# Performance work log

Measured on AMD Instinct MI355X. Metric: run time of the kernel, lower is better.

Reference implementation:

```python
import jax, jax.numpy as jnp
import numpy as np

N = 8_000_000   # hits
P = 100_000     # particle ids (0 = noise)


def setup_inputs() -> dict:
    key = jax.random.key(0)
    k1, k2, k3, k4, k5 = jax.random.split(key, 5)
    return {
        "w": jax.random.uniform(k1, (N,), dtype=jnp.float32),
        "beta": jax.random.uniform(k2, (N,), dtype=jnp.float32),
        "x": jax.random.normal(k3, (N, 3), dtype=jnp.float32),
        "y": jax.random.normal(k4, (N,), dtype=jnp.float32),
        "particle_id": jax.random.randint(k5, (N,), 0, P),
        "num_pids": P,
    }


def reference(w, beta, x, y, particle_id, num_pids):
    # BackgroundLoss.forward: only beta and particle_id matter; sb = 0.1.
    sb = jnp.asarray(0.1, beta.dtype)
    pid = particle_id

    # Per-particle max beta (segmented max replaces the per-pid argmax loop).
    counts = jax.ops.segment_sum(jnp.ones_like(beta), pid, num_segments=num_pids)
    max_beta = jax.ops.segment_max(beta, pid, num_segments=num_pids)

    # torch.unique(particle_id[particle_id > 0]) -> pids > 0 that actually occur.
    seg_ids = jnp.arange(num_pids)
    valid = (counts > 0) & (seg_ids > 0)
    n_valid = jnp.maximum(jnp.sum(valid), 1)
    attractive = jnp.sum(jnp.where(valid, 1.0 - max_beta, 0.0)) / n_valid.astype(beta.dtype)

    # Noise (pid == 0) term: sb * sum(n * beta) / nb.
    noise_mask = (pid == 0).astype(beta.dtype)
    nb = jnp.sum(noise_mask)
    noise = sb * jnp.sum(noise_mask * beta) / jnp.maximum(nb, 1.0)

    # If there are no noise hits the original returns 0.
    return jnp.where(nb == 0, jnp.asarray(0.0, beta.dtype), attractive + noise)
```

## Files before the change

### kernel.cpp

```cpp
#include <hip/hip_runtime.h>


#define ACC_NOISE  0
#define ACC_NB     1
#define ACC_ATTR   2
#define ACC_NVALID 3

#define RANGE_BITS_BIG 15
#define RANGE_BIG      (1 << RANGE_BITS_BIG)
#define NRANGE_BIG     4
#define TPB_BIG        1024

#define RANGE_BITS 14
#define RANGE      (1 << RANGE_BITS)
#define NRANGE     8
#define TPB        512

#define BPR        64

__global__ void bg_init_acc(float* __restrict__ acc) {
    if (threadIdx.x < 4) acc[threadIdx.x] = 0.0f;
}


__global__ __launch_bounds__(TPB_BIG) void bg_main_big(
        const float* __restrict__ beta, const int* __restrict__ pid,
        float* __restrict__ acc, unsigned int* __restrict__ slabs, int n) {
    extern __shared__ unsigned int tbl[];
    const int r = blockIdx.x / BPR;
    const int b = blockIdx.x % BPR;
    const int lo = r << RANGE_BITS_BIG;

    for (int i = threadIdx.x; i < RANGE_BIG; i += TPB_BIG) tbl[i] = 0u;
    __syncthreads();

    float noise_local = 0.0f;
    int nb_local = 0;

    const int n4 = n >> 2;
    const float4* __restrict__ b4 = (const float4*)beta;
    const int4* __restrict__ p4 = (const int4*)pid;
    const int gtid = b * TPB_BIG + (int)threadIdx.x;
    const int gstride = BPR * TPB_BIG;

    auto proc = [&](int p, float v) {
        int d = p - lo;
        if ((unsigned)d < (unsigned)RANGE_BIG) {
            if (p == 0) {
                noise_local += v;
                nb_local += 1;
            } else {
                unsigned int bits = __float_as_uint(v) + 1u;
                if (bits > tbl[d]) atomicMax(&tbl[d], bits);
            }
        }
    };

    int i = gtid;
    for (; i + gstride < n4; i += 2 * gstride) {
        float4 bb0 = b4[i];           int4 pp0 = p4[i];
        float4 bb1 = b4[i + gstride]; int4 pp1 = p4[i + gstride];
        proc(pp0.x, bb0.x); proc(pp0.y, bb0.y);
        proc(pp0.z, bb0.z); proc(pp0.w, bb0.w);
        proc(pp1.x, bb1.x); proc(pp1.y, bb1.y);
        proc(pp1.z, bb1.z); proc(pp1.w, bb1.w);
    }
    if (i < n4) {
        float4 bb = b4[i]; int4 pp = p4[i];
        proc(pp.x, bb.x); proc(pp.y, bb.y);
        proc(pp.z, bb.z); proc(pp.w, bb.w);
    }
    if (b == 0) {
        for (int t = (n4 << 2) + (int)threadIdx.x; t < n; t += TPB_BIG)
            proc(pid[t], beta[t]);
    }

    #pragma unroll
    for (int off = 32; off > 0; off >>= 1) {
        noise_local += __shfl_down(noise_local, off);
        nb_local    += __shfl_down(nb_local, off);
    }
    if ((threadIdx.x & 63) == 0 && nb_local != 0) {
        atomicAdd(&acc[ACC_NOISE], noise_local);
        atomicAdd(&acc[ACC_NB], (float)nb_local);
    }

    __syncthreads();
    uint4* __restrict__ o4 = (uint4*)(slabs + (size_t)blockIdx.x * RANGE_BIG);
    const uint4* __restrict__ t4 = (const uint4*)tbl;
    for (int k = threadIdx.x; k < RANGE_BIG / 4; k += TPB_BIG) o4[k] = t4[k];
}


__global__ __launch_bounds__(TPB) void bg_main_lds(
        const float* __restrict__ beta, const int* __restrict__ pid,
        float* __restrict__ acc, unsigned int* __restrict__ slabs, int n) {
    __shared__ unsigned int tbl[RANGE];
    const int r = blockIdx.x / BPR;
    const int b = blockIdx.x % BPR;
    const int lo = r << RANGE_BITS;

    for (int i = threadIdx.x; i < RANGE; i += TPB) tbl[i] = 0u;
    __syncthreads();

    float noise_local = 0.0f;
    int nb_local = 0;

    const int n4 = n >> 2;
    const float4* __restrict__ b4 = (const float4*)beta;
    const int4* __restrict__ p4 = (const int4*)pid;
    const int gtid = b * TPB + (int)threadIdx.x;
    const int gstride = BPR * TPB;

    auto proc = [&](int p, float v) {
        int d = p - lo;
        if ((unsigned)d < (unsigned)RANGE) {
            if (p == 0) {
                noise_local += v;
                nb_local += 1;
            } else {
                unsigned int bits = __float_as_uint(v) + 1u;
                if (bits > tbl[d]) atomicMax(&tbl[d], bits);
            }
        }
    };

    int i = gtid;
    for (; i + gstride < n4; i += 2 * gstride) {
        float4 bb0 = b4[i];           int4 pp0 = p4[i];
        float4 bb1 = b4[i + gstride]; int4 pp1 = p4[i + gstride];
        proc(pp0.x, bb0.x); proc(pp0.y, bb0.y);
        proc(pp0.z, bb0.z); proc(pp0.w, bb0.w);
        proc(pp1.x, bb1.x); proc(pp1.y, bb1.y);
        proc(pp1.z, bb1.z); proc(pp1.w, bb1.w);
    }
    if (i < n4) {
        float4 bb = b4[i]; int4 pp = p4[i];
        proc(pp.x, bb.x); proc(pp.y, bb.y);
        proc(pp.z, bb.z); proc(pp.w, bb.w);
    }
    if (b == 0) {
        for (int t = (n4 << 2) + (int)threadIdx.x; t < n; t += TPB)
            proc(pid[t], beta[t]);
    }

    #pragma unroll
    for (int off = 32; off > 0; off >>= 1) {
        noise_local += __shfl_down(noise_local, off);
        nb_local    += __shfl_down(nb_local, off);
    }
    if ((threadIdx.x & 63) == 0 && nb_local != 0) {
        atomicAdd(&acc[ACC_NOISE], noise_local);
        atomicAdd(&acc[ACC_NB], (float)nb_local);
    }

    __syncthreads();
    uint4* __restrict__ o4 = (uint4*)(slabs + (size_t)blockIdx.x * RANGE);
    const uint4* __restrict__ t4 = (const uint4*)tbl;
    for (int k = threadIdx.x; k < RANGE / 4; k += TPB) o4[k] = t4[k];
}


template <int RBITS>
__global__ __launch_bounds__(256) void bg_reduce_slab_t(
        const unsigned int* __restrict__ slabs, float* __restrict__ acc,
        const int* __restrict__ num_pids_p) {
    const int RSZ = 1 << RBITS;
    const int P = *num_pids_p;
    const int t = blockIdx.x * 256 + (int)threadIdx.x;
    const int e = t & (RSZ - 1);
    const int r = t >> RBITS;

    unsigned int v = 0u;
    const unsigned int* __restrict__ base =
        slabs + (size_t)(r * BPR) * RSZ + e;
    #pragma unroll 4
    for (int b = 0; b < BPR; ++b) {
        unsigned int u = base[(size_t)b * RSZ];
        v = (u > v) ? u : v;
    }

    const int p = (r << RBITS) | e;
    float s = 0.0f;
    int c = 0;
    if (p > 0 && p < P && v != 0u) {
        s = 1.0f - __uint_as_float(v - 1u);
        c = 1;
    }
    #pragma unroll
    for (int off = 32; off > 0; off >>= 1) {
        s += __shfl_down(s, off);
        c += __shfl_down(c, off);
    }
    if ((threadIdx.x & 63) == 0 && (c != 0 || s != 0.0f)) {
        atomicAdd(&acc[ACC_ATTR], s);
        atomicAdd(&acc[ACC_NVALID], (float)c);
    }
}


__global__ void bg_init(float* __restrict__ acc,
                        unsigned int* __restrict__ max_bits,
                        const int* __restrict__ num_pids_p) {
    const int P = *num_pids_p;
    const int gstride = gridDim.x * blockDim.x;
    const int tid = blockIdx.x * blockDim.x + threadIdx.x;
    if (tid < 4) acc[tid] = 0.0f;
    for (int i = tid; i < P; i += gstride) max_bits[i] = 0u;
}

__global__ void bg_main(const float* __restrict__ beta,
                        const int* __restrict__ pid,
                        float* __restrict__ acc,
                        unsigned int* __restrict__ max_bits, int n) {
    const int gstride = gridDim.x * blockDim.x;
    const int tid = blockIdx.x * blockDim.x + threadIdx.x;
    const int n4 = n >> 2;
    float noise_local = 0.0f;
    int nb_local = 0;
    auto proc = [&](int p, float b) {
        if (p == 0) { noise_local += b; nb_local += 1; }
        else {
            unsigned int bits = __float_as_uint(b) + 1u;
            if (bits > max_bits[p]) atomicMax(&max_bits[p], bits);
        }
    };
    const float4* __restrict__ b4 = (const float4*)beta;
    const int4* __restrict__ p4 = (const int4*)pid;
    for (int i = tid; i < n4; i += gstride) {
        float4 b = b4[i]; int4 p = p4[i];
        proc(p.x, b.x); proc(p.y, b.y); proc(p.z, b.z); proc(p.w, b.w);
    }
    for (int i = (n4 << 2) + tid; i < n; i += gstride)
        proc(pid[i], beta[i]);
    #pragma unroll
    for (int off = 32; off > 0; off >>= 1) {
        noise_local += __shfl_down(noise_local, off);
        nb_local    += __shfl_down(nb_local, off);
    }
    if ((threadIdx.x & 63) == 0 && nb_local != 0) {
        atomicAdd(&acc[ACC_NOISE], noise_local);
        atomicAdd(&acc[ACC_NB], (float)nb_local);
    }
}

__global__ void bg_reduce(const unsigned int* __restrict__ max_bits,
                          float* __restrict__ acc,
                          const int* __restrict__ num_pids_p) {
    const int P = *num_pids_p;
    const int gstride = gridDim.x * blockDim.x;
    float s = 0.0f;
    int c = 0;
    for (int i = blockIdx.x * blockDim.x + threadIdx.x; i < P; i += gstride) {
        if (i == 0) continue;
        unsigned int v = max_bits[i];
        if (v != 0u) { s += 1.0f - __uint_as_float(v - 1u); c += 1; }
    }
    #pragma unroll
    for (int off = 32; off > 0; off >>= 1) {
        s += __shfl_down(s, off);
        c += __shfl_down(c, off);
    }
    if ((threadIdx.x & 63) == 0 && (c != 0 || s != 0.0f)) {
        atomicAdd(&acc[ACC_ATTR], s);
        atomicAdd(&acc[ACC_NVALID], (float)c);
    }
}


__global__ void bg_finalize(const float* __restrict__ acc,
                            float* __restrict__ out) {
    float nb = acc[ACC_NB];
    float n_valid = fmaxf(acc[ACC_NVALID], 1.0f);
    float attractive = acc[ACC_ATTR] / n_valid;
    float noise = 0.1f * acc[ACC_NOISE] / fmaxf(nb, 1.0f);
    out[0] = (nb == 0.0f) ? 0.0f : (attractive + noise);
}

extern "C" void kernel_launch(void* const* d_in, const int* in_sizes, int n_in,
                              void* d_out, int out_size, void* d_ws, size_t ws_size,
                              hipStream_t stream) {
    const float* beta = (const float*)d_in[1];
    const int* pid = (const int*)d_in[4];
    const int* num_pids_p = (const int*)d_in[5];
    const int n = in_sizes[1];

    float* acc = (float*)d_ws;
    float* out = (float*)d_out;

    const size_t slab_bytes = (size_t)NRANGE * BPR * RANGE * sizeof(unsigned int);

    if (ws_size >= 16 + slab_bytes) {
        unsigned int* slabs = (unsigned int*)((char*)d_ws + 16);

        bool big = (hipFuncSetAttribute(
                        (const void*)bg_main_big,
                        hipFuncAttributeMaxDynamicSharedMemorySize,
                        RANGE_BIG * (int)sizeof(unsigned int)) == hipSuccess);

        bg_init_acc<<<1, 64, 0, stream>>>(acc);
        if (big) {
            bg_main_big<<<NRANGE_BIG * BPR, TPB_BIG,
                          RANGE_BIG * sizeof(unsigned int), stream>>>(
                beta, pid, acc, slabs, n);
            bg_reduce_slab_t<RANGE_BITS_BIG>
                <<<(NRANGE_BIG * RANGE_BIG) / 256, 256, 0, stream>>>(
                    slabs, acc, num_pids_p);
        } else {
            bg_main_lds<<<NRANGE * BPR, TPB, 0, stream>>>(beta, pid, acc, slabs, n);
            bg_reduce_slab_t<RANGE_BITS>
                <<<(NRANGE * RANGE) / 256, 256, 0, stream>>>(
                    slabs, acc, num_pids_p);
        }
        bg_finalize<<<1, 1, 0, stream>>>(acc, out);
    } else {
        unsigned int* max_bits = (unsigned int*)((char*)d_ws + 16);
        bg_init<<<512, 256, 0, stream>>>(acc, max_bits, num_pids_p);
        bg_main<<<2048, 256, 0, stream>>>(beta, pid, acc, max_bits, n);
        bg_reduce<<<512, 256, 0, stream>>>(max_bits, acc, num_pids_p);
        bg_finalize<<<1, 1, 0, stream>>>(acc, out);
    }
}
```

Measured before the change: 249.1 us.

## Cut pid ranges from four to three by folding tail range into range zero

Adds a new path that splits the pid space into three 32K ranges instead of four. The small tail above 3*32K (up to 4096 ids) is handled in an extra LDS table owned by the range-0 blocks. It raises blocks per range to 85 so all 255 blocks still cover the device. The goal is fewer full passes over the beta/pid arrays, since each range reads the whole input. In exchange range-0 blocks do more per-element work and LDS use grows, and the tail table silently assumes num_pids is at most 3*32768+4096.

```diff
diff --git a/kernel.cpp b/kernel.cpp
--- a/kernel.cpp
+++ b/kernel.cpp
@@ -6,20 +6,161 @@
 #define ACC_ATTR   2
 #define ACC_NVALID 3
 
-#define RANGE_BITS_BIG 15
-#define RANGE_BIG      (1 << RANGE_BITS_BIG)
-#define NRANGE_BIG     4
-#define TPB_BIG        1024
+#define RB          15
+#define RANGE_BIG   (1 << RB)
+#define NR_MAIN     3
+#define HI_BASE     (NR_MAIN << RB)
+#define HI_RANGE    4096
+#define BPR_BIG     85
+#define TPB_BIG     1024
+
+#define NRANGE_BIG  4
+#define BPR         64
 
 #define RANGE_BITS 14
 #define RANGE      (1 << RANGE_BITS)
 #define NRANGE     8
 #define TPB        512
 
-#define BPR        64
-
 __global__ void bg_init_acc(float* __restrict__ acc) {
     if (threadIdx.x < 4) acc[threadIdx.x] = 0.0f;
+}
+
+
+__global__ __launch_bounds__(TPB_BIG) void bg_main_r3(
+        const float* __restrict__ beta, const int* __restrict__ pid,
+        float* __restrict__ acc, unsigned int* __restrict__ slabs,
+        unsigned int* __restrict__ hi_slabs, int n) {
+    extern __shared__ unsigned int tbl[];
+    unsigned int* __restrict__ hi = tbl + RANGE_BIG;
+    const int r = blockIdx.x / BPR_BIG;
+    const int b = blockIdx.x % BPR_BIG;
+    const int lo = r << RB;
+
+    for (int i = threadIdx.x; i < RANGE_BIG + HI_RANGE; i += TPB_BIG) tbl[i] = 0u;
+    __syncthreads();
+
+    float noise_local = 0.0f;
+    int nb_local = 0;
+
+    const int n4 = n >> 2;
+    const float4* __restrict__ b4 = (const float4*)beta;
+    const int4* __restrict__ p4 = (const int4*)pid;
+    const int gtid = b * TPB_BIG + (int)threadIdx.x;
+    const int gstride = BPR_BIG * TPB_BIG;
+
+    auto stream = [&](auto&& proc) {
+        int i = gtid;
+        for (; i + gstride < n4; i += 2 * gstride) {
+            float4 bb0 = b4[i];           int4 pp0 = p4[i];
+            float4 bb1 = b4[i + gstride]; int4 pp1 = p4[i + gstride];
+            proc(pp0.x, bb0.x); proc(pp0.y, bb0.y);
+            proc(pp0.z, bb0.z); proc(pp0.w, bb0.w);
+            proc(pp1.x, bb1.x); proc(pp1.y, bb1.y);
+            proc(pp1.z, bb1.z); proc(pp1.w, bb1.w);
+        }
+        if (i < n4) {
+            float4 bb = b4[i]; int4 pp = p4[i];
+            proc(pp.x, bb.x); proc(pp.y, bb.y);
+            proc(pp.z, bb.z); proc(pp.w, bb.w);
+        }
+    };
+
+    if (r == 0) {
+        auto proc0 = [&](int p, float v) {
+            if (p == 0) { noise_local += v; nb_local += 1; return; }
+            unsigned int bits = __float_as_uint(v) + 1u;
+            if ((unsigned)p < (unsigned)RANGE_BIG) {
+                if (bits > tbl[p]) atomicMax(&tbl[p], bits);
+            } else {
+                int d = p - HI_BASE;
+                if ((unsigned)d < (unsigned)HI_RANGE)
+                    if (bits > hi[d]) atomicMax(&hi[d], bits);
+            }
+        };
+        stream(proc0);
+        if (b == 0) {
+            for (int t = (n4 << 2) + (int)threadIdx.x; t < n; t += TPB_BIG)
+                proc0(pid[t], beta[t]);
+        }
+    } else {
+        auto proc = [&](int p, float v) {
+            int d = p - lo;
+            if ((unsigned)d < (unsigned)RANGE_BIG) {
+                unsigned int bits = __float_as_uint(v) + 1u;
+                if (bits > tbl[d]) atomicMax(&tbl[d], bits);
+            }
+        };
+        stream(proc);
+    }
+
+    #pragma unroll
+    for (int off = 32; off > 0; off >>= 1) {
+        noise_local += __shfl_down(noise_local, off);
+        nb_local    += __shfl_down(nb_local, off);
+    }
+    if ((threadIdx.x & 63) == 0 && nb_local != 0) {
+        atomicAdd(&acc[ACC_NOISE], noise_local);
+        atomicAdd(&acc[ACC_NB], (float)nb_local);
+    }
+
+    __syncthreads();
+    uint4* __restrict__ o4 = (uint4*)(slabs + (size_t)blockIdx.x * RANGE_BIG);
+    const uint4* __restrict__ t4 = (const uint4*)tbl;
+    for (int k = threadIdx.x; k < RANGE_BIG / 4; k += TPB_BIG) o4[k] = t4[k];
+    if (r == 0) {
+        uint4* __restrict__ h4 = (uint4*)(hi_slabs + (size_t)b * HI_RANGE);
+        const uint4* __restrict__ hs4 = (const uint4*)hi;
+        for (int k = threadIdx.x; k < HI_RANGE / 4; k += TPB_BIG) h4[k] = hs4[k];
+    }
+}
+
+__global__ __launch_bounds__(256) void bg_reduce_r3(
+        const unsigned int* __restrict__ slabs,
+        const unsigned int* __restrict__ hi_slabs,
+        float* __restrict__ acc, const int* __restrict__ num_pids_p) {
+    const int P = *num_pids_p;
+    const int t = blockIdx.x * 256 + (int)threadIdx.x;
+
+    unsigned int v = 0u;
+    int p;
+    if (t < NR_MAIN * RANGE_BIG) {
+        const int e = t & (RANGE_BIG - 1);
+        const int r = t >> RB;
+        const unsigned int* __restrict__ base =
+            slabs + (size_t)(r * BPR_BIG) * RANGE_BIG + e;
+        #pragma unroll 5
+        for (int b = 0; b < BPR_BIG; ++b) {
+            unsigned int u = base[(size_t)b * RANGE_BIG];
+            v = (u > v) ? u : v;
+        }
+        p = t;
+    } else {
+        const int e = t - NR_MAIN * RANGE_BIG;
+        const unsigned int* __restrict__ base = hi_slabs + e;
+        #pragma unroll 5
+        for (int b = 0; b < BPR_BIG; ++b) {
+            unsigned int u = base[(size_t)b * HI_RANGE];
+            v = (u > v) ? u : v;
+        }
+        p = HI_BASE + e;
+    }
+
+    float s = 0.0f;
+    int c = 0;
+    if (p > 0 && p < P && v != 0u) {
+        s = 1.0f - __uint_as_float(v - 1u);
+        c = 1;
+    }
+    #pragma unroll
+    for (int off = 32; off > 0; off >>= 1) {
+        s += __shfl_down(s, off);
+        c += __shfl_down(c, off);
+    }
+    if ((threadIdx.x & 63) == 0 && (c != 0 || s != 0.0f)) {
+        atomicAdd(&acc[ACC_ATTR], s);
+        atomicAdd(&acc[ACC_NVALID], (float)c);
+    }
 }
 
 
@@ -29,7 +170,7 @@
     extern __shared__ unsigned int tbl[];
     const int r = blockIdx.x / BPR;
     const int b = blockIdx.x % BPR;
-    const int lo = r << RANGE_BITS_BIG;
+    const int lo = r << RB;
 
     for (int i = threadIdx.x; i < RANGE_BIG; i += TPB_BIG) tbl[i] = 0u;
     __syncthreads();
@@ -288,9 +429,28 @@
     float* acc = (float*)d_ws;
     float* out = (float*)d_out;
 
-    const size_t slab_bytes = (size_t)NRANGE * BPR * RANGE * sizeof(unsigned int);
-
-    if (ws_size >= 16 + slab_bytes) {
+    const size_t slab_r3_main = (size_t)NR_MAIN * BPR_BIG * RANGE_BIG * sizeof(unsigned int);
+    const size_t slab_r3_hi   = (size_t)BPR_BIG * HI_RANGE * sizeof(unsigned int);
+    const size_t slab_r3      = slab_r3_main + slab_r3_hi;
+    const size_t slab_big = (size_t)NRANGE_BIG * BPR * RANGE_BIG * sizeof(unsigned int);
+    const size_t slab_sm  = (size_t)NRANGE * BPR * RANGE * sizeof(unsigned int);
+
+    if (ws_size >= 16 + slab_r3 &&
+        hipFuncSetAttribute((const void*)bg_main_r3,
+                            hipFuncAttributeMaxDynamicSharedMemorySize,
+                            (RANGE_BIG + HI_RANGE) * (int)sizeof(unsigned int))
+            == hipSuccess) {
+        unsigned int* slabs = (unsigned int*)((char*)d_ws + 16);
+        unsigned int* hi_slabs = slabs + (size_t)NR_MAIN * BPR_BIG * RANGE_BIG;
+
+        bg_init_acc<<<1, 64, 0, stream>>>(acc);
+        bg_main_r3<<<NR_MAIN * BPR_BIG, TPB_BIG,
+                     (RANGE_BIG + HI_RANGE) * sizeof(unsigned int), stream>>>(
+            beta, pid, acc, slabs, hi_slabs, n);
+        bg_reduce_r3<<<(NR_MAIN * RANGE_BIG + HI_RANGE) / 256, 256, 0, stream>>>(
+            slabs, hi_slabs, acc, num_pids_p);
+        bg_finalize<<<1, 1, 0, stream>>>(acc, out);
+    } else if (ws_size >= 16 + slab_big) {
         unsigned int* slabs = (unsigned int*)((char*)d_ws + 16);
 
         bool big = (hipFuncSetAttribute(
@@ -303,7 +463,7 @@
             bg_main_big<<<NRANGE_BIG * BPR, TPB_BIG,
                           RANGE_BIG * sizeof(unsigned int), stream>>>(
                 beta, pid, acc, slabs, n);
-            bg_reduce_slab_t<RANGE_BITS_BIG>
+            bg_reduce_slab_t<RB>
                 <<<(NRANGE_BIG * RANGE_BIG) / 256, 256, 0, stream>>>(
                     slabs, acc, num_pids_p);
         } else {
```

Result: slower. 256.4 us (+2.9%).
